# Performance work log

Measured on AMD Instinct MI355X. Metric: run time of the kernel, lower is better.

Reference implementation:

```python
import jax, jax.numpy as jnp
import numpy as np

B, L, F, H, U = 512, 64, 2048, 512, 512


def setup_inputs() -> dict:
    key = jax.random.key(0)
    ks = jax.random.split(key, 10)
    s = 0.05
    return {
        'features': jax.random.normal(ks[0], (B, L, F), jnp.float32),
        'hidden': jax.random.normal(ks[1], (B, H), jnp.float32),
        'W1': jax.random.normal(ks[2], (F, U), jnp.float32) * s,
        'b1': jnp.zeros((U,), jnp.float32),
        'W2': jax.random.normal(ks[3], (H, U), jnp.float32) * s,
        'b2': jnp.zeros((U,), jnp.float32),
        'V': jax.random.normal(ks[4], (U, 1), jnp.float32) * s,
        'bV': jnp.zeros((1,), jnp.float32),
        'W3': jax.random.normal(ks[5], (F + H, U), jnp.float32) * s,
        'b3': jnp.zeros((U,), jnp.float32),
        'ka1': jax.random.normal(ks[6], (H, L), jnp.float32) * s,
        'kb1': jax.random.normal(ks[7], (L, L), jnp.float32) * s,
        'ka2': jax.random.normal(ks[8], (H, L), jnp.float32) * s,
        'kb2': jax.random.normal(ks[9], (L, L), jnp.float32) * s,
    }


def reference(features, hidden, W1, b1, W2, b2, V, bV, W3, b3, ka1, kb1, ka2, kb2):
    # features: [B, L, F], hidden: [B, H]
    Lp = features.shape[1]
    h = hidden[:, None, :]  # [B, 1, H] = hidden_with_time_axis

    # score_model == 'default'
    score = jnp.tanh(features @ W1 + b1 + (h @ W2 + b2))  # [B, L, U]
    logits = score @ V + bV  # [B, L, 1]
    attention_weights = jax.nn.softmax(logits, axis=1)  # [B, L, 1]

    # local_att == 'True': Gaussian window re-weighting (vectorized version of
    # the original nested Python loops over (batch, position)).
    def local_p(ka, kb):
        t = jnp.tanh(h @ ka) @ kb  # [B, 1, L]
        t = jax.nn.sigmoid(t) * jnp.sqrt(jnp.float32(Lp))
        return jnp.transpose(t, (0, 2, 1))  # [B, L, 1]

    p1 = local_p(ka1, kb1)  # predicted row center, [B, L, 1]
    p2 = local_p(ka2, kb2)  # predicted col center, [B, L, 1]

    i = jnp.arange(Lp, dtype=jnp.float32)
    g = jnp.sqrt(jnp.float32(Lp))
    rows = jnp.floor((i + 1.0) / g)                 # s_t[..., 0]
    cols = jnp.floor(jnp.mod(i + 1.0, g)) - 1.0     # s_t[..., 1]
    d2 = (rows[None, :, None] - p1) ** 2 + (cols[None, :, None] - p2) ** 2  # [B, L, 1]

    D = 1.0
    attention_weights = attention_weights * jnp.exp(-d2 / (0.5 * D * D))

    context_vector = jnp.sum(attention_weights * features, axis=1)  # [B, F]

    # context_vector_concat == 'True'
    out = jnp.tanh(jnp.concatenate([context_vector, hidden], axis=-1)) @ W3 + b3  # [B, U]
    return out, attention_weights
```

## Files before the change

kernel.cpp:

```cpp
#include <hip/hip_runtime.h>

typedef __bf16 bf16x8 __attribute__((ext_vector_type(8)));
typedef float f32x4 __attribute__((ext_vector_type(4)));

static __device__ __forceinline__ unsigned short f2bf(float f) {
  union { float fv; unsigned u; } v; v.fv = f;
  unsigned u = v.u;
  u += 0x7fffu + ((u >> 16) & 1u);
  return (unsigned short)(u >> 16);
}

__global__ __launch_bounds__(256) void pack_all(
    const float* __restrict__ W1, const float* __restrict__ W2,
    const float* __restrict__ W3,
    unsigned short* __restrict__ W1p, unsigned short* __restrict__ W2p,
    unsigned short* __restrict__ W3p) {
  __shared__ float tile[32][65];
  const int N = 512;
  const float* W; unsigned short* P; int nk;
  if (blockIdx.z == 0)      { W = W1; P = W1p; nk = 64; }
  else if (blockIdx.z == 1) { W = W2; P = W2p; nk = 16; }
  else                      { W = W3; P = W3p; nk = 80; }
  if ((int)blockIdx.x >= nk) return;
  int k0 = blockIdx.x * 32, n0 = blockIdx.y * 64;
  int t = threadIdx.x;
  int nn = t & 63, kkb = t >> 6;
#pragma unroll
  for (int i = 0; i < 8; ++i) {
    int kk = kkb + i * 4;
    tile[kk][nn] = W[(size_t)(k0 + kk) * N + n0 + nn];
  }
  __syncthreads();
  size_t base = (size_t)blockIdx.x * (N * 32) + (size_t)n0 * 32;
#pragma unroll
  for (int i = 0; i < 8; ++i) {
    int e = t + i * 256;
    P[base + e] = f2bf(tile[e & 31][e >> 5]);
  }
}

__global__ __launch_bounds__(128) void prep_batch(
    const float* __restrict__ hidden,
    const float* __restrict__ ka1, const float* __restrict__ kb1,
    const float* __restrict__ ka2, const float* __restrict__ kb2,
    float* __restrict__ gauss,
    unsigned short* __restrict__ hid_bf,
    unsigned short* __restrict__ A2) {
  int b = blockIdx.x, t = threadIdx.x;
  __shared__ float hl[512];
  __shared__ float tt[128];
  __shared__ float pp[128];
  for (int i = t; i < 512; i += 128) {
    float v = hidden[b * 512 + i];
    hl[i] = v;
    hid_bf[b * 512 + i] = f2bf(v);
    A2[(size_t)b * 2560 + 2048 + i] = f2bf(tanhf(v));
  }
  __syncthreads();
  {
    const float* ka = (t < 64) ? ka1 : ka2;
    int lp = t & 63;
    float s0 = 0.f, s1 = 0.f, s2 = 0.f, s3 = 0.f;
    for (int h = 0; h < 512; h += 4) {
      s0 += hl[h + 0] * ka[(h + 0) * 64 + lp];
      s1 += hl[h + 1] * ka[(h + 1) * 64 + lp];
      s2 += hl[h + 2] * ka[(h + 2) * 64 + lp];
      s3 += hl[h + 3] * ka[(h + 3) * 64 + lp];
    }
    tt[t] = tanhf((s0 + s1) + (s2 + s3));
  }
  __syncthreads();
  {
    const float* kb = (t < 64) ? kb1 : kb2;
    const float* ts = (t < 64) ? tt : tt + 64;
    int l = t & 63;
    float s = 0.f;
    for (int j = 0; j < 64; ++j) s += ts[j] * kb[j * 64 + l];
    pp[t] = 8.0f / (1.0f + expf(-s));
  }
  __syncthreads();
  if (t < 64) {
    float fi = (float)(t + 1);
    float r = floorf(fi * 0.125f);
    float c = floorf(fmodf(fi, 8.0f)) - 1.0f;
    float dr = r - pp[t], dc = c - pp[64 + t];
    gauss[b * 64 + t] = expf(-2.0f * (dr * dr + dc * dc));
  }
}

__global__ __launch_bounds__(256, 4) void gemm64(
    const unsigned short* __restrict__ A, int K,
    const unsigned short* __restrict__ Wp,
    const float* __restrict__ bias,
    float* __restrict__ C) {
  __shared__ unsigned short lA[64 * 40];
  __shared__ unsigned short lB[64 * 40];
  int m0 = blockIdx.x * 64, n0 = blockIdx.y * 64;
  int t = threadIdx.x;
  int w = t >> 6, lane = t & 63, q = lane >> 4, l15 = lane & 15;
  f32x4 acc[4] = {};
  int arow = t >> 2, achk = (t & 3) * 8;
  int nsteps = K >> 5;
  const unsigned short* pA = A + (size_t)(m0 + arow) * K + achk;
  const unsigned short* pB = Wp + (size_t)n0 * 32 + t * 8;
  float bsv = bias[n0 + w * 16 + l15];
  int4 av = *(const int4*)(pA);
  int4 bvv = *(const int4*)(pB);
  for (int ks = 0; ks < nsteps; ++ks) {
    __syncthreads();
    *(int4*)(lA + arow * 40 + achk) = av;
    *(int4*)(lB + arow * 40 + achk) = bvv;
    __syncthreads();
    int ksn = (ks + 1 < nsteps) ? ks + 1 : ks;
    av = *(const int4*)(pA + ksn * 32);
    bvv = *(const int4*)(pB + (size_t)ksn * (512 * 32));
    bf16x8 bf = *(const bf16x8*)(lB + (w * 16 + l15) * 40 + q * 8);
#pragma unroll
    for (int mt = 0; mt < 4; ++mt) {
      bf16x8 af = *(const bf16x8*)(lA + (mt * 16 + l15) * 40 + q * 8);
      acc[mt] = __builtin_amdgcn_mfma_f32_16x16x32_bf16(af, bf, acc[mt], 0, 0, 0);
    }
  }
#pragma unroll
  for (int mt = 0; mt < 4; ++mt)
#pragma unroll
    for (int j = 0; j < 4; ++j)
      C[(size_t)(m0 + mt * 16 + q * 4 + j) * 512 + n0 + w * 16 + l15] = acc[mt][j] + bsv;
}

__global__ __launch_bounds__(512, 4) void attn_main(
    const float* __restrict__ feat,
    const unsigned short* __restrict__ W1p,
    const float* __restrict__ b1,
    const float* __restrict__ hb,
    const float* __restrict__ V,
    const float* __restrict__ bVp,
    const float* __restrict__ gauss,
    float* __restrict__ aw_out,
    unsigned short* __restrict__ A2) {
  __shared__ unsigned short lA[64 * 40];
  __shared__ unsigned short lB[512 * 40];
  __shared__ float red[64 * 8];
  __shared__ float awl[64];
  int b = blockIdx.x, t = threadIdx.x;
  int w = t >> 6, lane = t & 63, q = lane >> 4, l15 = lane & 15;
  f32x4 acc[4][4] = {};
  int arow = t >> 3, achk = t & 7;
  const float* Ab = feat + (size_t)b * (64 * 2048);
  const float* pA = Ab + (size_t)arow * 2048 + achk * 4;
  const unsigned short* pB = W1p + (size_t)t * 8;

  float vv[4], bb[4];
#pragma unroll
  for (int nt = 0; nt < 4; ++nt) {
    int u = w * 64 + nt * 16 + l15;
    vv[nt] = V[u];
    bb[nt] = b1[u] + hb[b * 512 + u];
  }
  float gs = (t < 64) ? gauss[b * 64 + t] : 0.f;
  float bV0 = bVp[0];

  float4 av = *(const float4*)(pA);
  int4 bv0 = *(const int4*)(pB);
  int4 bv1 = *(const int4*)(pB + 4096);
  int4 bv2 = *(const int4*)(pB + 8192);
  int4 bv3 = *(const int4*)(pB + 12288);

  for (int ks = 0; ks < 64; ++ks) {
    __syncthreads();
    ushort4 a4;
    a4.x = f2bf(av.x); a4.y = f2bf(av.y); a4.z = f2bf(av.z); a4.w = f2bf(av.w);
    *(ushort4*)(lA + arow * 40 + achk * 4) = a4;
    {
      int c = t;
      *(int4*)(lB + (c >> 2) * 40 + (c & 3) * 8) = bv0;
      c = t + 512;
      *(int4*)(lB + (c >> 2) * 40 + (c & 3) * 8) = bv1;
      c = t + 1024;
      *(int4*)(lB + (c >> 2) * 40 + (c & 3) * 8) = bv2;
      c = t + 1536;
      *(int4*)(lB + (c >> 2) * 40 + (c & 3) * 8) = bv3;
    }
    __syncthreads();
    {
      int ksn = (ks < 63) ? ks + 1 : ks;
      const unsigned short* bp = pB + (size_t)ksn * (512 * 32);
      av  = *(const float4*)(pA + ksn * 32);
      bv0 = *(const int4*)(bp);
      bv1 = *(const int4*)(bp + 4096);
      bv2 = *(const int4*)(bp + 8192);
      bv3 = *(const int4*)(bp + 12288);
    }
    bf16x8 bf[4];
#pragma unroll
    for (int nt = 0; nt < 4; ++nt)
      bf[nt] = *(const bf16x8*)(lB + (w * 64 + nt * 16 + l15) * 40 + q * 8);
#pragma unroll
    for (int mt = 0; mt < 4; ++mt) {
      bf16x8 af = *(const bf16x8*)(lA + (mt * 16 + l15) * 40 + q * 8);
#pragma unroll
      for (int nt = 0; nt < 4; ++nt)
        acc[mt][nt] = __builtin_amdgcn_mfma_f32_16x16x32_bf16(af, bf[nt], acc[mt][nt], 0, 0, 0);
    }
  }
#pragma unroll
  for (int mt = 0; mt < 4; ++mt) {
#pragma unroll
    for (int j = 0; j < 4; ++j) {
      float p = 0.f;
#pragma unroll
      for (int nt = 0; nt < 4; ++nt)
        p += tanhf(acc[mt][nt][j] + bb[nt]) * vv[nt];
      p += __shfl_xor(p, 1);
      p += __shfl_xor(p, 2);
      p += __shfl_xor(p, 4);
      p += __shfl_xor(p, 8);
      if (l15 == 0) red[(mt * 16 + q * 4 + j) * 8 + w] = p;
    }
  }
  __syncthreads();
  if (t < 64) {
    float s = bV0;
#pragma unroll
    for (int ww = 0; ww < 8; ++ww) s += red[t * 8 + ww];
    float mx = s;
#pragma unroll
    for (int o = 1; o < 64; o <<= 1) mx = fmaxf(mx, __shfl_xor(mx, o));
    float e = expf(s - mx);
    float sm = e;
#pragma unroll
    for (int o = 1; o < 64; o <<= 1) sm += __shfl_xor(sm, o);
    float a = (e / sm) * gs;
    awl[t] = a;
    aw_out[b * 64 + t] = a;
  }
  __syncthreads();
  float4 cacc = make_float4(0.f, 0.f, 0.f, 0.f);
  for (int l = 0; l < 64; ++l) {
    float a = awl[l];
    float4 fv = *(const float4*)(Ab + (size_t)l * 2048 + t * 4);
    cacc.x += a * fv.x; cacc.y += a * fv.y; cacc.z += a * fv.z; cacc.w += a * fv.w;
  }
  ushort4 o4;
  o4.x = f2bf(tanhf(cacc.x)); o4.y = f2bf(tanhf(cacc.y));
  o4.z = f2bf(tanhf(cacc.z)); o4.w = f2bf(tanhf(cacc.w));
  *(ushort4*)(A2 + (size_t)b * 2560 + t * 4) = o4;
}

extern "C" void kernel_launch(void* const* d_in, const int* in_sizes, int n_in,
                              void* d_out, int out_size, void* d_ws, size_t ws_size,
                              hipStream_t stream) {
  (void)in_sizes; (void)n_in; (void)out_size; (void)ws_size;
  const float* feat   = (const float*)d_in[0];
  const float* hidden = (const float*)d_in[1];
  const float* W1  = (const float*)d_in[2];
  const float* b1  = (const float*)d_in[3];
  const float* W2  = (const float*)d_in[4];
  const float* b2  = (const float*)d_in[5];
  const float* V   = (const float*)d_in[6];
  const float* bV  = (const float*)d_in[7];
  const float* W3  = (const float*)d_in[8];
  const float* b3  = (const float*)d_in[9];
  const float* ka1 = (const float*)d_in[10];
  const float* kb1 = (const float*)d_in[11];
  const float* ka2 = (const float*)d_in[12];
  const float* kb2 = (const float*)d_in[13];

  char* ws = (char*)d_ws;
  unsigned short* W1p   = (unsigned short*)(ws);
  unsigned short* W2p   = (unsigned short*)(ws + 2097152);
  unsigned short* W3p   = (unsigned short*)(ws + 2621440);
  unsigned short* hidbf = (unsigned short*)(ws + 5242880);
  float*          hb    = (float*)(ws + 5767168);
  float*          gauss = (float*)(ws + 6815744);
  unsigned short* A2    = (unsigned short*)(ws + 6946816);

  float* out    = (float*)d_out;
  float* aw_out = out + 512 * 512;

  pack_all<<<dim3(80, 8, 3), 256, 0, stream>>>(W1, W2, W3, W1p, W2p, W3p);
  prep_batch<<<512, 128, 0, stream>>>(hidden, ka1, kb1, ka2, kb2, gauss, hidbf, A2);
  gemm64<<<dim3(8, 8), 256, 0, stream>>>(hidbf, 512, W2p, b2, hb);
  attn_main<<<512, 512, 0, stream>>>(feat, W1p, b1, hb, V, bV, gauss, aw_out, A2);
  gemm64<<<dim3(8, 8), 256, 0, stream>>>(A2, 2560, W3p, b3, out);
}
```

Before: 542.9 us.

## Repack weights to MFMA fragment layout, register-resident B tiles, split-K final GEMM

Weights are repacked into a k8-major layout so each lane loads its MFMA B fragment straight from global memory, which removes the LDS staging of W1/W2/W3. attn_main moves to 256 threads, each wave covering 128 columns with a double-buffered A tile in shared memory, and tanh/exp switch to fast exp-based versions. The final W3 GEMM becomes a 4-way split-K followed by a reduction kernel, to expose more blocks. The trade-offs are higher register pressure, an extra kernel launch, and some extra traffic for the partial sums.

Result: faster. 507.8 us (-6.5%).

```diff
diff --git a/kernel.cpp b/kernel.cpp
--- a/kernel.cpp
+++ b/kernel.cpp
@@ -8,6 +8,12 @@
   unsigned u = v.u;
   u += 0x7fffu + ((u >> 16) & 1u);
   return (unsigned short)(u >> 16);
+}
+
+static __device__ __forceinline__ float fast_tanh(float x) {
+  x = fminf(fmaxf(x, -15.f), 15.f);
+  float ex = __expf(2.f * x);
+  return (ex - 1.f) / (ex + 1.f);
 }
 
 __global__ __launch_bounds__(256) void pack_all(
@@ -31,11 +37,12 @@
     tile[kk][nn] = W[(size_t)(k0 + kk) * N + n0 + nn];
   }
   __syncthreads();
-  size_t base = (size_t)blockIdx.x * (N * 32) + (size_t)n0 * 32;
 #pragma unroll
   for (int i = 0; i < 8; ++i) {
     int e = t + i * 256;
-    P[base + e] = f2bf(tile[e & 31][e >> 5]);
+    int k8 = e & 7, n = (e >> 3) & 63, c = e >> 9;
+    size_t dst = (size_t)((k0 >> 3) + c) * 4096 + (size_t)(n0 + n) * 8 + k8;
+    P[dst] = f2bf(tile[c * 8 + k8][n]);
   }
 }
 
@@ -88,47 +95,76 @@
   }
 }
 
-__global__ __launch_bounds__(256, 4) void gemm64(
-    const unsigned short* __restrict__ A, int K,
+__global__ __launch_bounds__(256, 4) void gemm64d(
+    const unsigned short* __restrict__ A, int lda, int k8_stride, int nsteps,
     const unsigned short* __restrict__ Wp,
     const float* __restrict__ bias,
     float* __restrict__ C) {
   __shared__ unsigned short lA[64 * 40];
-  __shared__ unsigned short lB[64 * 40];
   int m0 = blockIdx.x * 64, n0 = blockIdx.y * 64;
+  int z = blockIdx.z;
+  int k8 = z * k8_stride;
   int t = threadIdx.x;
   int w = t >> 6, lane = t & 63, q = lane >> 4, l15 = lane & 15;
   f32x4 acc[4] = {};
   int arow = t >> 2, achk = (t & 3) * 8;
-  int nsteps = K >> 5;
-  const unsigned short* pA = A + (size_t)(m0 + arow) * K + achk;
-  const unsigned short* pB = Wp + (size_t)n0 * 32 + t * 8;
-  float bsv = bias[n0 + w * 16 + l15];
+  const unsigned short* pA = A + (size_t)(m0 + arow) * lda + (size_t)k8 * 8 + achk;
+  const unsigned short* pB = Wp + ((size_t)(k8 + q) * 512 + n0 + w * 16 + l15) * 8;
   int4 av = *(const int4*)(pA);
-  int4 bvv = *(const int4*)(pB);
+  int4 bv = *(const int4*)(pB);
   for (int ks = 0; ks < nsteps; ++ks) {
     __syncthreads();
     *(int4*)(lA + arow * 40 + achk) = av;
-    *(int4*)(lB + arow * 40 + achk) = bvv;
     __syncthreads();
     int ksn = (ks + 1 < nsteps) ? ks + 1 : ks;
     av = *(const int4*)(pA + ksn * 32);
-    bvv = *(const int4*)(pB + (size_t)ksn * (512 * 32));
-    bf16x8 bf = *(const bf16x8*)(lB + (w * 16 + l15) * 40 + q * 8);
+    int4 bn = *(const int4*)(pB + (size_t)ksn * 16384);
+    bf16x8 bf = *(const bf16x8*)&bv;
 #pragma unroll
     for (int mt = 0; mt < 4; ++mt) {
       bf16x8 af = *(const bf16x8*)(lA + (mt * 16 + l15) * 40 + q * 8);
       acc[mt] = __builtin_amdgcn_mfma_f32_16x16x32_bf16(af, bf, acc[mt], 0, 0, 0);
     }
-  }
-#pragma unroll
-  for (int mt = 0; mt < 4; ++mt)
-#pragma unroll
-    for (int j = 0; j < 4; ++j)
-      C[(size_t)(m0 + mt * 16 + q * 4 + j) * 512 + n0 + w * 16 + l15] = acc[mt][j] + bsv;
-}
-
-__global__ __launch_bounds__(512, 4) void attn_main(
+    bv = bn;
+  }
+  int col = n0 + w * 16 + l15;
+  if (bias) {
+    float bsv = bias[col];
+#pragma unroll
+    for (int mt = 0; mt < 4; ++mt)
+#pragma unroll
+      for (int j = 0; j < 4; ++j)
+        C[(size_t)(m0 + mt * 16 + q * 4 + j) * 512 + col] = acc[mt][j] + bsv;
+  } else {
+    float* Cp = C + (size_t)z * 262144;
+#pragma unroll
+    for (int mt = 0; mt < 4; ++mt)
+#pragma unroll
+      for (int j = 0; j < 4; ++j)
+        Cp[(size_t)(m0 + mt * 16 + q * 4 + j) * 512 + col] = acc[mt][j];
+  }
+}
+
+__global__ __launch_bounds__(256) void reduce4(const float* __restrict__ part,
+                                               const float* __restrict__ b3,
+                                               float* __restrict__ out) {
+  int i = blockIdx.x * 256 + threadIdx.x;
+  int base = i * 4;
+  int n = base & 511;
+  float4 p0 = *(const float4*)(part + base);
+  float4 p1 = *(const float4*)(part + 262144 + base);
+  float4 p2 = *(const float4*)(part + 524288 + base);
+  float4 p3 = *(const float4*)(part + 786432 + base);
+  float4 bv = *(const float4*)(b3 + n);
+  float4 r;
+  r.x = p0.x + p1.x + p2.x + p3.x + bv.x;
+  r.y = p0.y + p1.y + p2.y + p3.y + bv.y;
+  r.z = p0.z + p1.z + p2.z + p3.z + bv.z;
+  r.w = p0.w + p1.w + p2.w + p3.w + bv.w;
+  *(float4*)(out + base) = r;
+}
+
+__global__ __launch_bounds__(256, 2) void attn_main(
     const float* __restrict__ feat,
     const unsigned short* __restrict__ W1p,
     const float* __restrict__ b1,
@@ -138,95 +174,114 @@
     const float* __restrict__ gauss,
     float* __restrict__ aw_out,
     unsigned short* __restrict__ A2) {
-  __shared__ unsigned short lA[64 * 40];
-  __shared__ unsigned short lB[512 * 40];
-  __shared__ float red[64 * 8];
+  __shared__ unsigned short lA[2][64 * 40];
+  __shared__ float red[64 * 4];
   __shared__ float awl[64];
   int b = blockIdx.x, t = threadIdx.x;
   int w = t >> 6, lane = t & 63, q = lane >> 4, l15 = lane & 15;
-  f32x4 acc[4][4] = {};
-  int arow = t >> 3, achk = t & 7;
+  f32x4 acc[4][8] = {};
+  int row0 = t >> 3, ch0 = t & 7;
   const float* Ab = feat + (size_t)b * (64 * 2048);
-  const float* pA = Ab + (size_t)arow * 2048 + achk * 4;
-  const unsigned short* pB = W1p + (size_t)t * 8;
-
-  float vv[4], bb[4];
-#pragma unroll
-  for (int nt = 0; nt < 4; ++nt) {
-    int u = w * 64 + nt * 16 + l15;
+  const float* pA0 = Ab + row0 * 2048 + ch0 * 4;
+  const float* pA1 = pA0 + 32 * 2048;
+  const unsigned short* pB = W1p + ((size_t)q * 512 + w * 128 + l15) * 8;
+  int wA = row0 * 40 + ch0 * 4;
+
+  float vv[8], bb[8];
+#pragma unroll
+  for (int nt = 0; nt < 8; ++nt) {
+    int u = w * 128 + nt * 16 + l15;
     vv[nt] = V[u];
     bb[nt] = b1[u] + hb[b * 512 + u];
   }
   float gs = (t < 64) ? gauss[b * 64 + t] : 0.f;
   float bV0 = bVp[0];
 
-  float4 av = *(const float4*)(pA);
-  int4 bv0 = *(const int4*)(pB);
-  int4 bv1 = *(const int4*)(pB + 4096);
-  int4 bv2 = *(const int4*)(pB + 8192);
-  int4 bv3 = *(const int4*)(pB + 12288);
-
-  for (int ks = 0; ks < 64; ++ks) {
+  auto mmaStep = [&](int buf, const int4* B) {
+#pragma unroll
+    for (int mt = 0; mt < 4; ++mt) {
+      bf16x8 af = *(const bf16x8*)(&lA[buf][(mt * 16 + l15) * 40 + q * 8]);
+#pragma unroll
+      for (int nt = 0; nt < 8; ++nt)
+        acc[mt][nt] = __builtin_amdgcn_mfma_f32_16x16x32_bf16(
+            af, *(const bf16x8*)&B[nt], acc[mt][nt], 0, 0, 0);
+    }
+  };
+  auto stage = [&](int buf, const float4& x0, const float4& x1) {
+    ushort4 u0, u1;
+    u0.x = f2bf(x0.x); u0.y = f2bf(x0.y); u0.z = f2bf(x0.z); u0.w = f2bf(x0.w);
+    u1.x = f2bf(x1.x); u1.y = f2bf(x1.y); u1.z = f2bf(x1.z); u1.w = f2bf(x1.w);
+    *(ushort4*)(&lA[buf][wA]) = u0;
+    *(ushort4*)(&lA[buf][wA + 1280]) = u1;
+  };
+
+  int4 bc[8], bn[8];
+  float4 a0, a1, na0, na1;
+  a0 = *(const float4*)(pA0);
+  a1 = *(const float4*)(pA1);
+#pragma unroll
+  for (int nt = 0; nt < 8; ++nt) bc[nt] = *(const int4*)(pB + nt * 128);
+  stage(0, a0, a1);
+  na0 = *(const float4*)(pA0 + 32);
+  na1 = *(const float4*)(pA1 + 32);
+#pragma unroll
+  for (int nt = 0; nt < 8; ++nt) bn[nt] = *(const int4*)(pB + 16384 + nt * 128);
+  __syncthreads();
+
+  for (int s2 = 0; s2 < 32; ++s2) {
+    int s = 2 * s2;
+    stage(1, na0, na1);
+    {
+      int kf = (s + 2 < 64) ? s + 2 : 63;
+      a0 = *(const float4*)(pA0 + kf * 32);
+      a1 = *(const float4*)(pA1 + kf * 32);
+    }
+    mmaStep(0, bc);
+    {
+      int kf = (s + 2 < 64) ? s + 2 : 63;
+      const unsigned short* bp = pB + (size_t)kf * 16384;
+#pragma unroll
+      for (int nt = 0; nt < 8; ++nt) bc[nt] = *(const int4*)(bp + nt * 128);
+    }
     __syncthreads();
-    ushort4 a4;
-    a4.x = f2bf(av.x); a4.y = f2bf(av.y); a4.z = f2bf(av.z); a4.w = f2bf(av.w);
-    *(ushort4*)(lA + arow * 40 + achk * 4) = a4;
+    stage(0, a0, a1);
     {
-      int c = t;
-      *(int4*)(lB + (c >> 2) * 40 + (c & 3) * 8) = bv0;
-      c = t + 512;
-      *(int4*)(lB + (c >> 2) * 40 + (c & 3) * 8) = bv1;
-      c = t + 1024;
-      *(int4*)(lB + (c >> 2) * 40 + (c & 3) * 8) = bv2;
-      c = t + 1536;
-      *(int4*)(lB + (c >> 2) * 40 + (c & 3) * 8) = bv3;
+      int kf = (s + 3 < 64) ? s + 3 : 63;
+      na0 = *(const float4*)(pA0 + kf * 32);
+      na1 = *(const float4*)(pA1 + kf * 32);
+    }
+    mmaStep(1, bn);
+    {
+      int kf = (s + 3 < 64) ? s + 3 : 63;
+      const unsigned short* bp = pB + (size_t)kf * 16384;
+#pragma unroll
+      for (int nt = 0; nt < 8; ++nt) bn[nt] = *(const int4*)(bp + nt * 128);
     }
     __syncthreads();
-    {
-      int ksn = (ks < 63) ? ks + 1 : ks;
-      const unsigned short* bp = pB + (size_t)ksn * (512 * 32);
-      av  = *(const float4*)(pA + ksn * 32);
-      bv0 = *(const int4*)(bp);
-      bv1 = *(const int4*)(bp + 4096);
-      bv2 = *(const int4*)(bp + 8192);
-      bv3 = *(const int4*)(bp + 12288);
-    }
-    bf16x8 bf[4];
-#pragma unroll
-    for (int nt = 0; nt < 4; ++nt)
-      bf[nt] = *(const bf16x8*)(lB + (w * 64 + nt * 16 + l15) * 40 + q * 8);
-#pragma unroll
-    for (int mt = 0; mt < 4; ++mt) {
-      bf16x8 af = *(const bf16x8*)(lA + (mt * 16 + l15) * 40 + q * 8);
-#pragma unroll
-      for (int nt = 0; nt < 4; ++nt)
-        acc[mt][nt] = __builtin_amdgcn_mfma_f32_16x16x32_bf16(af, bf[nt], acc[mt][nt], 0, 0, 0);
-    }
-  }
+  }
+
 #pragma unroll
   for (int mt = 0; mt < 4; ++mt) {
 #pragma unroll
     for (int j = 0; j < 4; ++j) {
       float p = 0.f;
 #pragma unroll
-      for (int nt = 0; nt < 4; ++nt)
-        p += tanhf(acc[mt][nt][j] + bb[nt]) * vv[nt];
+      for (int nt = 0; nt < 8; ++nt)
+        p += fast_tanh(acc[mt][nt][j] + bb[nt]) * vv[nt];
       p += __shfl_xor(p, 1);
       p += __shfl_xor(p, 2);
       p += __shfl_xor(p, 4);
       p += __shfl_xor(p, 8);
-      if (l15 == 0) red[(mt * 16 + q * 4 + j) * 8 + w] = p;
+      if (l15 == 0) red[(mt * 16 + q * 4 + j) * 4 + w] = p;
     }
   }
   __syncthreads();
   if (t < 64) {
-    float s = bV0;
-#pragma unroll
-    for (int ww = 0; ww < 8; ++ww) s += red[t * 8 + ww];
+    float s = bV0 + red[t * 4] + red[t * 4 + 1] + red[t * 4 + 2] + red[t * 4 + 3];
     float mx = s;
 #pragma unroll
     for (int o = 1; o < 64; o <<= 1) mx = fmaxf(mx, __shfl_xor(mx, o));
-    float e = expf(s - mx);
+    float e = __expf(s - mx);
     float sm = e;
 #pragma unroll
     for (int o = 1; o < 64; o <<= 1) sm += __shfl_xor(sm, o);
@@ -235,16 +290,23 @@
     aw_out[b * 64 + t] = a;
   }
   __syncthreads();
-  float4 cacc = make_float4(0.f, 0.f, 0.f, 0.f);
+  float4 c0 = make_float4(0.f, 0.f, 0.f, 0.f);
+  float4 c1 = make_float4(0.f, 0.f, 0.f, 0.f);
+  const float* pF = Ab + t * 8;
   for (int l = 0; l < 64; ++l) {
     float a = awl[l];
-    float4 fv = *(const float4*)(Ab + (size_t)l * 2048 + t * 4);
-    cacc.x += a * fv.x; cacc.y += a * fv.y; cacc.z += a * fv.z; cacc.w += a * fv.w;
-  }
-  ushort4 o4;
-  o4.x = f2bf(tanhf(cacc.x)); o4.y = f2bf(tanhf(cacc.y));
-  o4.z = f2bf(tanhf(cacc.z)); o4.w = f2bf(tanhf(cacc.w));
-  *(ushort4*)(A2 + (size_t)b * 2560 + t * 4) = o4;
+    float4 f0 = *(const float4*)(pF + l * 2048);
+    float4 f1 = *(const float4*)(pF + l * 2048 + 4);
+    c0.x += a * f0.x; c0.y += a * f0.y; c0.z += a * f0.z; c0.w += a * f0.w;
+    c1.x += a * f1.x; c1.y += a * f1.y; c1.z += a * f1.z; c1.w += a * f1.w;
+  }
+  ushort4 o0, o1;
+  o0.x = f2bf(fast_tanh(c0.x)); o0.y = f2bf(fast_tanh(c0.y));
+  o0.z = f2bf(fast_tanh(c0.z)); o0.w = f2bf(fast_tanh(c0.w));
+  o1.x = f2bf(fast_tanh(c1.x)); o1.y = f2bf(fast_tanh(c1.y));
+  o1.z = f2bf(fast_tanh(c1.z)); o1.w = f2bf(fast_tanh(c1.w));
+  *(ushort4*)(A2 + (size_t)b * 2560 + t * 8) = o0;
+  *(ushort4*)(A2 + (size_t)b * 2560 + t * 8 + 4) = o1;
 }
 
 extern "C" void kernel_launch(void* const* d_in, const int* in_sizes, int n_in,
@@ -267,20 +329,22 @@
   const float* kb2 = (const float*)d_in[13];
 
   char* ws = (char*)d_ws;
-  unsigned short* W1p   = (unsigned short*)(ws);
-  unsigned short* W2p   = (unsigned short*)(ws + 2097152);
-  unsigned short* W3p   = (unsigned short*)(ws + 2621440);
-  unsigned short* hidbf = (unsigned short*)(ws + 5242880);
-  float*          hb    = (float*)(ws + 5767168);
-  float*          gauss = (float*)(ws + 6815744);
-  unsigned short* A2    = (unsigned short*)(ws + 6946816);
+  unsigned short* W3p   = (unsigned short*)(ws);
+  unsigned short* A2    = (unsigned short*)(ws + 2621440);
+  unsigned short* W1p   = (unsigned short*)(ws + 5242880);
+  unsigned short* W2p   = (unsigned short*)(ws + 7340032);
+  unsigned short* hidbf = (unsigned short*)(ws + 7864320);
+  float*          hb    = (float*)(ws + 8388608);
+  float*          gauss = (float*)(ws + 9437184);
+  float*          part  = (float*)(ws + 5242880);
 
   float* out    = (float*)d_out;
   float* aw_out = out + 512 * 512;
 
   pack_all<<<dim3(80, 8, 3), 256, 0, stream>>>(W1, W2, W3, W1p, W2p, W3p);
   prep_batch<<<512, 128, 0, stream>>>(hidden, ka1, kb1, ka2, kb2, gauss, hidbf, A2);
-  gemm64<<<dim3(8, 8), 256, 0, stream>>>(hidbf, 512, W2p, b2, hb);
-  attn_main<<<512, 512, 0, stream>>>(feat, W1p, b1, hb, V, bV, gauss, aw_out, A2);
-  gemm64<<<dim3(8, 8), 256, 0, stream>>>(A2, 2560, W3p, b3, out);
-}
+  gemm64d<<<dim3(8, 8, 1), 256, 0, stream>>>(hidbf, 512, 0, 16, W2p, b2, hb);
+  attn_main<<<512, 256, 0, stream>>>(feat, W1p, b1, hb, V, bV, gauss, aw_out, A2);
+  gemm64d<<<dim3(8, 8, 4), 256, 0, stream>>>(A2, 2560, 80, 20, W3p, nullptr, part);
+  reduce4<<<256, 256, 0, stream>>>(part, b3, out);
+}
```
